# Optimization experiments

Hardware: AMD Instinct MI355X
Metric: run time of the kernel (lower is better)

Reference implementation:

```python
import jax, jax.numpy as jnp
import numpy as np

B, T, C, H = 8, 1024, 1024, 16
D = C // H  # head_dim = 64


def setup_inputs() -> dict:
    key = jax.random.key(0)
    k1, k2, k3 = jax.random.split(key, 3)
    x = jax.random.normal(k1, (B, T, C), dtype=jnp.float32)
    # boolean causal mask: True = attend (PyTorch SDPA bool-mask semantics)
    attn_mask = jnp.tril(jnp.ones((T, T), dtype=jnp.bool_))[None, None, :, :]
    w_attn = jax.random.normal(k2, (C, 3 * C), dtype=jnp.float32) * (1.0 / np.sqrt(C))
    b_attn = jnp.zeros((3 * C,), dtype=jnp.float32)
    w_proj = jax.random.normal(k3, (C, C), dtype=jnp.float32) * (1.0 / np.sqrt(C))
    b_proj = jnp.zeros((C,), dtype=jnp.float32)
    return {"x": x, "attn_mask": attn_mask, "w_attn": w_attn, "b_attn": b_attn,
            "w_proj": w_proj, "b_proj": b_proj}


def reference(x, attn_mask, w_attn, b_attn, w_proj, b_proj):
    Bx, Tx, Cx = x.shape
    qkv = x @ w_attn + b_attn                      # [B,T,3C]
    q, k, v = jnp.split(qkv, 3, axis=-1)
    # [B,T,C] -> [B,H,T,D]
    q = q.reshape(Bx, Tx, H, D).transpose(0, 2, 1, 3)
    k = k.reshape(Bx, Tx, H, D).transpose(0, 2, 1, 3)
    v = v.reshape(Bx, Tx, H, D).transpose(0, 2, 1, 3)
    scale = 1.0 / jnp.sqrt(jnp.asarray(D, dtype=x.dtype))
    scores = jnp.einsum('bhqd,bhkd->bhqk', q, k) * scale  # [B,H,T,T]
    neg = jnp.asarray(jnp.finfo(x.dtype).min, dtype=x.dtype)
    scores = jnp.where(attn_mask, scores, neg)
    probs = jax.nn.softmax(scores, axis=-1)
    y = jnp.einsum('bhqk,bhkd->bhqd', probs, v)    # [B,H,T,D]
    y = y.transpose(0, 2, 1, 3).reshape(Bx, Tx, Cx)
    return y @ w_proj + b_proj
```

## Files before the change

kernel.cpp:

```cpp
#include <hip/hip_runtime.h>


typedef __bf16 bf16x8 __attribute__((ext_vector_type(8)));
typedef float f32x4 __attribute__((ext_vector_type(4)));
typedef unsigned uint4e __attribute__((ext_vector_type(4)));
typedef unsigned short ushort8e __attribute__((ext_vector_type(8)));

typedef __attribute__((address_space(1))) const unsigned as1_u32;
typedef __attribute__((address_space(3))) unsigned as3_u32;

#define NEG_INF (-__builtin_inff())

__device__ __forceinline__ unsigned short f2bf(float f) {
  unsigned u = __builtin_bit_cast(unsigned, f);
  u += 0x7fffu + ((u >> 16) & 1u);
  return (unsigned short)(u >> 16);
}


__global__ void cvt_x_kernel(const float* __restrict__ in, unsigned short* __restrict__ out) {
  size_t i = (size_t)(blockIdx.x * 256 + threadIdx.x) * 8;
  float4 a = *(const float4*)(in + i);
  float4 b = *(const float4*)(in + i + 4);
  ushort8e o;
  o[0] = f2bf(a.x); o[1] = f2bf(a.y); o[2] = f2bf(a.z); o[3] = f2bf(a.w);
  o[4] = f2bf(b.x); o[5] = f2bf(b.y); o[6] = f2bf(b.z); o[7] = f2bf(b.w);
  *(ushort8e*)(out + i) = o;
}

__global__ void cvt_wT_kernel(const float* __restrict__ w, unsigned short* __restrict__ wT,
                              int K, int N) {
  __shared__ float tile[32][33];
  const int n0 = blockIdx.x * 32, k0 = blockIdx.y * 32;
  const int tx = threadIdx.x, ty = threadIdx.y;
#pragma unroll
  for (int i = 0; i < 32; i += 8)
    tile[ty + i][tx] = w[(size_t)(k0 + ty + i) * N + n0 + tx];
  __syncthreads();
#pragma unroll
  for (int i = 0; i < 32; i += 8)
    wT[(size_t)(n0 + ty + i) * K + k0 + tx] = f2bf(tile[tx][ty + i]);
}


template <int EPI, int BNT>
__global__ __launch_bounds__(512, 2) void gemm_kernel(
    const unsigned short* __restrict__ A, const unsigned short* __restrict__ BT,
    const float* __restrict__ bias, float* __restrict__ outF,
    unsigned short* __restrict__ qO, unsigned short* __restrict__ kO,
    unsigned short* __restrict__ vO, int M, int N, int K) {
  constexpr int WN = BNT / 4;
  constexpr int NREP = WN / 16;
  constexpr int BISS = BNT / 64;
  constexpr int ATILE = 256 * 64;
  constexpr int BTILE = BNT * 64;
  __shared__ __align__(16) unsigned short LDS[2][ATILE + BTILE];

  const int tid = threadIdx.x;
  const int w = tid >> 6, lane = tid & 63;
  const int g = lane >> 4, cx = lane & 15;
  const int bm = blockIdx.y * 256, bn = blockIdx.x * BNT;
  const int wm = (w >> 2) * 128;
  const int wn = (w & 3) * WN;
  const int NT = K >> 6;

  const int srow = w * 8 + (lane >> 3);
  const int schunk = ((lane & 7) ^ ((lane >> 3) & 7)) << 3;
  const unsigned short* gAr = A + (size_t)(bm + srow) * K + schunk;
  const unsigned short* gBr = BT + (size_t)(bn + srow) * K + schunk;

  auto stage = [&](int t, int buf) {
    const int ko = t * 64;
#pragma unroll
    for (int i = 0; i < 4; ++i)
      __builtin_amdgcn_global_load_lds(
          (as1_u32*)(const void*)(gAr + (size_t)i * 64 * K + ko),
          (as3_u32*)(void*)&LDS[buf][(i * 64 + w * 8) * 64], 16, 0, 0);
#pragma unroll
    for (int i = 0; i < BISS; ++i)
      __builtin_amdgcn_global_load_lds(
          (as1_u32*)(const void*)(gBr + (size_t)i * 64 * K + ko),
          (as3_u32*)(void*)&LDS[buf][ATILE + (i * 64 + w * 8) * 64], 16, 0, 0);
  };

  f32x4 acc[8][NREP] = {};
  const int rsw = cx & 7;

  stage(0, 0);
  asm volatile("s_waitcnt vmcnt(0)" ::: "memory");
  __builtin_amdgcn_s_barrier();
  asm volatile("" ::: "memory");

  for (int t = 0; t < NT; ++t) {
    const int buf = t & 1;
    if (t + 1 < NT) stage(t + 1, buf ^ 1);
    bf16x8 bfr[NREP][2];
#pragma unroll
    for (int nr = 0; nr < NREP; ++nr) {
      const int RB = wn + nr * 16 + cx;
#pragma unroll
      for (int ks = 0; ks < 2; ++ks)
        bfr[nr][ks] = *(const bf16x8*)&LDS[buf][ATILE + RB * 64 + (((ks * 4 + g) ^ rsw) << 3)];
    }
#pragma unroll
    for (int q = 0; q < 4; ++q) {
      bf16x8 af[2][2];
#pragma unroll
      for (int mr = 0; mr < 2; ++mr) {
        const int R = wm + q * 32 + mr * 16 + cx;
#pragma unroll
        for (int ks = 0; ks < 2; ++ks)
          af[mr][ks] = *(const bf16x8*)&LDS[buf][R * 64 + (((ks * 4 + g) ^ rsw) << 3)];
      }
      __builtin_amdgcn_s_setprio(1);
#pragma unroll
      for (int mr = 0; mr < 2; ++mr)
#pragma unroll
        for (int nr = 0; nr < NREP; ++nr)
#pragma unroll
          for (int ks = 0; ks < 2; ++ks)
            acc[q * 2 + mr][nr] = __builtin_amdgcn_mfma_f32_16x16x32_bf16(
                af[mr][ks], bfr[nr][ks], acc[q * 2 + mr][nr], 0, 0, 0);
      __builtin_amdgcn_s_setprio(0);
    }
    if (t + 1 < NT) {
      asm volatile("s_waitcnt vmcnt(0)" ::: "memory");
      __builtin_amdgcn_s_barrier();
      asm volatile("" ::: "memory");
    }
  }

  if (EPI == 0) {
#pragma unroll
    for (int q = 0; q < 4; ++q)
#pragma unroll
      for (int mr = 0; mr < 2; ++mr) {
        const int m0 = bm + wm + q * 32 + mr * 16 + (g << 2);
        const int b = m0 >> 10, t0 = m0 & 1023;
#pragma unroll
        for (int nr = 0; nr < NREP; ++nr) {
          const int n = bn + wn + nr * 16 + cx;
          const float bv = bias[n];
          const int which = n >> 10, rem = n & 1023;
          const int h = rem >> 6, d = rem & 63;
          const int bh = b * 16 + h;
          f32x4& a4 = acc[q * 2 + mr][nr];
          if (which == 2) {
            uint2 pv;
            pv.x = (unsigned)f2bf(a4[0] + bv) | ((unsigned)f2bf(a4[1] + bv) << 16);
            pv.y = (unsigned)f2bf(a4[2] + bv) | ((unsigned)f2bf(a4[3] + bv) << 16);
            *(uint2*)(vO + ((size_t)bh * 64 + d) * 1024 + t0) = pv;
          } else {
            unsigned short* dst = (which == 0 ? qO : kO);
            const float scl = (which == 0) ? 0.18033688011112042f : 1.0f;
#pragma unroll
            for (int r = 0; r < 4; ++r)
              dst[((size_t)bh * 1024 + (t0 + r)) * 64 + d] = f2bf((a4[r] + bv) * scl);
          }
        }
      }
  } else {
#pragma unroll
    for (int q = 0; q < 4; ++q)
#pragma unroll
      for (int mr = 0; mr < 2; ++mr) {
        const int m0 = bm + wm + q * 32 + mr * 16 + (g << 2);
#pragma unroll
        for (int nr = 0; nr < NREP; ++nr) {
          const int n = bn + wn + nr * 16 + cx;
          const float bv = bias[n];
          f32x4& a4 = acc[q * 2 + mr][nr];
#pragma unroll
          for (int r = 0; r < 4; ++r)
            outF[(size_t)(m0 + r) * N + n] = a4[r] + bv;
        }
      }
  }
}


__global__ __launch_bounds__(256) void attn_kernel(
    const unsigned short* __restrict__ qB, const unsigned short* __restrict__ kB,
    const unsigned short* __restrict__ vB, unsigned short* __restrict__ yB) {
  __shared__ __align__(16) unsigned short Ks[2][64 * 64];
  __shared__ __align__(16) unsigned short Vs[2][64 * 64];
  const int lane = threadIdx.x & 63, w = threadIdx.x >> 6;
  const int g = lane >> 4, cx = lane & 15;
  const int bh = blockIdx.x;
  const int qt = 7 - blockIdx.y;
  const int qb0 = qt * 128;
  const int nt = qt * 2 + 2;
  const unsigned short* Qh = qB + (size_t)bh * 65536;
  const unsigned short* Kh = kB + (size_t)bh * 65536;
  const unsigned short* Vh = vB + (size_t)bh * 65536;

  const int qsb0 = qb0 + w * 16, qsb1 = qb0 + 64 + w * 16;

  bf16x8 qf[2][2];
#pragma unroll
  for (int s = 0; s < 2; ++s) {
    const int qq = (s ? qsb1 : qsb0) + cx;
#pragma unroll
    for (int h = 0; h < 2; ++h)
      qf[s][h] = *(const bf16x8*)(Qh + (size_t)qq * 64 + h * 32 + g * 8);
  }

  f32x4 oacc[2][4] = {};
  float mrun0 = NEG_INF, mrun1 = NEG_INF, L0 = 0.f, L1 = 0.f;

  const int srl = lane >> 3, sch = lane & 7;

  auto stage = [&](int t, int buf) {
#pragma unroll
    for (int i = 0; i < 2; ++i) {
      const int row = w * 16 + i * 8 + srl;
      const int csw = (sch ^ (row & 7)) << 3;
      const unsigned short* gk = Kh + (size_t)(t * 64 + row) * 64 + csw;
      __builtin_amdgcn_global_load_lds((as1_u32*)(const void*)gk,
          (as3_u32*)(void*)&Ks[buf][(w * 16 + i * 8) * 64], 16, 0, 0);
      const unsigned short* gv = Vh + (size_t)row * 1024 + t * 64 + csw;
      __builtin_amdgcn_global_load_lds((as1_u32*)(const void*)gv,
          (as3_u32*)(void*)&Vs[buf][(w * 16 + i * 8) * 64], 16, 0, 0);
    }
  };

  auto mkpf = [&](const float* pp) -> bf16x8 {
    unsigned lo0 = (unsigned)f2bf(pp[0]) | ((unsigned)f2bf(pp[1]) << 16);
    unsigned hi0 = (unsigned)f2bf(pp[2]) | ((unsigned)f2bf(pp[3]) << 16);
    unsigned lo1 = (unsigned)f2bf(pp[4]) | ((unsigned)f2bf(pp[5]) << 16);
    unsigned hi1 = (unsigned)f2bf(pp[6]) | ((unsigned)f2bf(pp[7]) << 16);
    const int s0 = ((g & 1) << 5) + cx, s1 = s0 + 16;
    unsigned a0 = __shfl(lo0, s0), a1 = __shfl(hi0, s0), a2 = __shfl(lo0, s1), a3 = __shfl(hi0, s1);
    unsigned b0 = __shfl(lo1, s0), b1 = __shfl(hi1, s0), b2 = __shfl(lo1, s1), b3 = __shfl(hi1, s1);
    const bool chh = g >= 2;
    uint4e pw;
    pw[0] = chh ? b0 : a0; pw[1] = chh ? b1 : a1; pw[2] = chh ? b2 : a2; pw[3] = chh ? b3 : a3;
    return __builtin_bit_cast(bf16x8, pw);
  };

  stage(0, 0);
  asm volatile("s_waitcnt vmcnt(0)" ::: "memory");
  __builtin_amdgcn_s_barrier();
  asm volatile("" ::: "memory");

  for (int t = 0; t < nt; ++t) {
    const int buf = t & 1;
    if (t + 1 < nt) stage(t + 1, buf ^ 1);
    const int k0 = t * 64;
    const bool act0 = k0 <= qsb0 + 15;

    bf16x8 kf[4][2];
#pragma unroll
    for (int kc = 0; kc < 4; ++kc) {
      const int row = kc * 16 + cx;
#pragma unroll
      for (int h = 0; h < 2; ++h)
        kf[kc][h] = *(const bf16x8*)&Ks[buf][row * 64 + (((h * 4 + g) ^ (row & 7)) << 3)];
    }
    f32x4 sa[2][4];
#pragma unroll
    for (int kc = 0; kc < 4; ++kc) {
      f32x4 z = {0.f, 0.f, 0.f, 0.f};
      sa[1][kc] = __builtin_amdgcn_mfma_f32_16x16x32_bf16(kf[kc][0], qf[1][0], z, 0, 0, 0);
      sa[1][kc] = __builtin_amdgcn_mfma_f32_16x16x32_bf16(kf[kc][1], qf[1][1], sa[1][kc], 0, 0, 0);
    }
    if (act0) {
#pragma unroll
      for (int kc = 0; kc < 4; ++kc) {
        f32x4 z = {0.f, 0.f, 0.f, 0.f};
        sa[0][kc] = __builtin_amdgcn_mfma_f32_16x16x32_bf16(kf[kc][0], qf[0][0], z, 0, 0, 0);
        sa[0][kc] = __builtin_amdgcn_mfma_f32_16x16x32_bf16(kf[kc][1], qf[0][1], sa[0][kc], 0, 0, 0);
      }
    }

    bf16x8 vf[4][2];
#pragma unroll
    for (int db = 0; db < 4; ++db) {
      const int row = db * 16 + cx;
#pragma unroll
      for (int h = 0; h < 2; ++h)
        vf[db][h] = *(const bf16x8*)&Vs[buf][row * 64 + (((h * 4 + g) ^ (row & 7)) << 3)];
    }

#pragma unroll
    for (int s = 0; s < 2; ++s) {
      if (s == 0 && !act0) continue;
      const int qsb = s ? qsb1 : qsb0;
      const int qg = qsb + cx;
      float& mrun = s ? mrun1 : mrun0;
      float& L = s ? L1 : L0;
      float p[16];
      const bool straddle = (k0 + 63) > qsb;
#pragma unroll
      for (int kc = 0; kc < 4; ++kc)
#pragma unroll
        for (int r = 0; r < 4; ++r) {
          float v = sa[s][kc][r];
          if (straddle && (k0 + kc * 16 + (g << 2) + r) > qg) v = NEG_INF;
          p[kc * 4 + r] = v;
        }
      float m01 = fmaxf(fmaxf(p[0], p[1]), fmaxf(p[2], p[3]));
      float m23 = fmaxf(fmaxf(p[4], p[5]), fmaxf(p[6], p[7]));
      float m45 = fmaxf(fmaxf(p[8], p[9]), fmaxf(p[10], p[11]));
      float m67 = fmaxf(fmaxf(p[12], p[13]), fmaxf(p[14], p[15]));
      float pm = fmaxf(fmaxf(m01, m23), fmaxf(m45, m67));
      pm = fmaxf(pm, __shfl_xor(pm, 16));
      pm = fmaxf(pm, __shfl_xor(pm, 32));
      const float mnew = fmaxf(mrun, pm);
      const float cs = __builtin_amdgcn_exp2f(mrun - mnew);
      mrun = mnew;
      float ps = 0.f;
#pragma unroll
      for (int e = 0; e < 16; ++e) {
        p[e] = __builtin_amdgcn_exp2f(p[e] - mnew);
        ps += p[e];
      }
      ps += __shfl_xor(ps, 16);
      ps += __shfl_xor(ps, 32);
      L = L * cs + ps;
#pragma unroll
      for (int db = 0; db < 4; ++db) {
        oacc[s][db][0] *= cs; oacc[s][db][1] *= cs;
        oacc[s][db][2] *= cs; oacc[s][db][3] *= cs;
      }
      const bf16x8 pf0 = mkpf(p);
      const bf16x8 pf1 = mkpf(p + 8);
#pragma unroll
      for (int db = 0; db < 4; ++db) {
        oacc[s][db] = __builtin_amdgcn_mfma_f32_16x16x32_bf16(vf[db][0], pf0, oacc[s][db], 0, 0, 0);
        oacc[s][db] = __builtin_amdgcn_mfma_f32_16x16x32_bf16(vf[db][1], pf1, oacc[s][db], 0, 0, 0);
      }
    }

    asm volatile("s_waitcnt vmcnt(0)" ::: "memory");
    __builtin_amdgcn_s_barrier();
    asm volatile("" ::: "memory");
  }

  const int b = bh >> 4, h = bh & 15;
#pragma unroll
  for (int s = 0; s < 2; ++s) {
    const float inv = 1.0f / (s ? L1 : L0);
    const int qg = (s ? qsb1 : qsb0) + cx;
    unsigned short* yp = yB + (size_t)(b * 1024 + qg) * 1024 + h * 64;
#pragma unroll
    for (int db = 0; db < 4; ++db) {
      uint2 pv;
      pv.x = (unsigned)f2bf(oacc[s][db][0] * inv) | ((unsigned)f2bf(oacc[s][db][1] * inv) << 16);
      pv.y = (unsigned)f2bf(oacc[s][db][2] * inv) | ((unsigned)f2bf(oacc[s][db][3] * inv) << 16);
      *(uint2*)(yp + db * 16 + (g << 2)) = pv;
    }
  }
}


extern "C" void kernel_launch(void* const* d_in, const int* in_sizes, int n_in,
                              void* d_out, int out_size, void* d_ws, size_t ws_size,
                              hipStream_t stream) {
  (void)in_sizes; (void)n_in; (void)out_size; (void)ws_size;
  const float* x = (const float*)d_in[0];
  const float* w_attn = (const float*)d_in[2];
  const float* b_attn = (const float*)d_in[3];
  const float* w_proj = (const float*)d_in[4];
  const float* b_proj = (const float*)d_in[5];
  float* out = (float*)d_out;

  char* ws = (char*)d_ws;
  unsigned short* xb     = (unsigned short*)(ws);
  unsigned short* wqkvT  = (unsigned short*)(ws + 16777216);
  unsigned short* wprojT = (unsigned short*)(ws + 23068672);
  unsigned short* qb     = (unsigned short*)(ws + 25165824);
  unsigned short* kb     = (unsigned short*)(ws + 41943040);
  unsigned short* vtb    = (unsigned short*)(ws + 58720256);
  unsigned short* yb     = (unsigned short*)(ws + 75497472);

  cvt_x_kernel<<<4096, 256, 0, stream>>>(x, xb);
  cvt_wT_kernel<<<dim3(96, 32), dim3(32, 8), 0, stream>>>(w_attn, wqkvT, 1024, 3072);
  cvt_wT_kernel<<<dim3(32, 32), dim3(32, 8), 0, stream>>>(w_proj, wprojT, 1024, 1024);

  gemm_kernel<0, 256><<<dim3(12, 32), 512, 0, stream>>>(xb, wqkvT, b_attn, nullptr,
                                                        qb, kb, vtb, 8192, 3072, 1024);
  attn_kernel<<<dim3(128, 8), 256, 0, stream>>>(qb, kb, vtb, yb);
  gemm_kernel<1, 128><<<dim3(8, 32), 512, 0, stream>>>(yb, wprojT, b_proj, out,
                                                       nullptr, nullptr, nullptr, 8192, 1024, 1024);
}
```

Measured before the change: 170.2 us.

## Triple-buffer GEMM K-loop, shrink QKV tile to 128 wide, remap blocks per XCD

Moves the GEMM from double buffering to a three-stage LDS ring with prefetch distance two and a partial vmcnt wait, so global loads overlap compute for longer. The QKV GEMM tile width drops from 256 to 128 (768 blocks) and a 1D grid is remapped so consecutive tiles land on the same XCD for L2 reuse. The trip count is hardcoded to 16, so K is fixed at 1024. LDS use grows to three buffers, which may limit occupancy, and each block does less work per B tile.

```diff
diff --git a/kernel.cpp b/kernel.cpp
--- a/kernel.cpp
+++ b/kernel.cpp
@@ -43,33 +43,36 @@
 }
 
 
-template <int EPI, int BNT>
+template <int EPI, int NTN>
 __global__ __launch_bounds__(512, 2) void gemm_kernel(
     const unsigned short* __restrict__ A, const unsigned short* __restrict__ BT,
     const float* __restrict__ bias, float* __restrict__ outF,
     unsigned short* __restrict__ qO, unsigned short* __restrict__ kO,
     unsigned short* __restrict__ vO, int M, int N, int K) {
-  constexpr int WN = BNT / 4;
-  constexpr int NREP = WN / 16;
-  constexpr int BISS = BNT / 64;
   constexpr int ATILE = 256 * 64;
-  constexpr int BTILE = BNT * 64;
-  __shared__ __align__(16) unsigned short LDS[2][ATILE + BTILE];
+  constexpr int BTILE = 128 * 64;
+  constexpr int NT = 16;
+  __shared__ __align__(16) unsigned short LDS[3][ATILE + BTILE];
 
   const int tid = threadIdx.x;
   const int w = tid >> 6, lane = tid & 63;
   const int g = lane >> 4, cx = lane & 15;
-  const int bm = blockIdx.y * 256, bn = blockIdx.x * BNT;
+
+  constexpr int CPX = NTN * 32 / 8;
+  const int bid = blockIdx.x;
+  const int wg = (bid & 7) * CPX + (bid >> 3);
+  const int bm = (wg / NTN) * 256, bn = (wg % NTN) * 128;
+
   const int wm = (w >> 2) * 128;
-  const int wn = (w & 3) * WN;
-  const int NT = K >> 6;
+  const int wn = (w & 3) * 32;
 
   const int srow = w * 8 + (lane >> 3);
   const int schunk = ((lane & 7) ^ ((lane >> 3) & 7)) << 3;
   const unsigned short* gAr = A + (size_t)(bm + srow) * K + schunk;
   const unsigned short* gBr = BT + (size_t)(bn + srow) * K + schunk;
 
-  auto stage = [&](int t, int buf) {
+  auto stage = [&](int t) {
+    const int buf = t % 3;
     const int ko = t * 64;
 #pragma unroll
     for (int i = 0; i < 4; ++i)
@@ -77,30 +80,33 @@
           (as1_u32*)(const void*)(gAr + (size_t)i * 64 * K + ko),
           (as3_u32*)(void*)&LDS[buf][(i * 64 + w * 8) * 64], 16, 0, 0);
 #pragma unroll
-    for (int i = 0; i < BISS; ++i)
+    for (int i = 0; i < 2; ++i)
       __builtin_amdgcn_global_load_lds(
           (as1_u32*)(const void*)(gBr + (size_t)i * 64 * K + ko),
           (as3_u32*)(void*)&LDS[buf][ATILE + (i * 64 + w * 8) * 64], 16, 0, 0);
   };
 
-  f32x4 acc[8][NREP] = {};
+  f32x4 acc[8][2] = {};
   const int rsw = cx & 7;
 
-  stage(0, 0);
-  asm volatile("s_waitcnt vmcnt(0)" ::: "memory");
-  __builtin_amdgcn_s_barrier();
-  asm volatile("" ::: "memory");
+  stage(0);
+  stage(1);
 
   for (int t = 0; t < NT; ++t) {
-    const int buf = t & 1;
-    if (t + 1 < NT) stage(t + 1, buf ^ 1);
-    bf16x8 bfr[NREP][2];
-#pragma unroll
-    for (int nr = 0; nr < NREP; ++nr) {
+    if (t + 1 < NT) asm volatile("s_waitcnt vmcnt(6)" ::: "memory");
+    else            asm volatile("s_waitcnt vmcnt(0)" ::: "memory");
+    __builtin_amdgcn_s_barrier();
+    asm volatile("" ::: "memory");
+    if (t + 2 < NT) stage(t + 2);
+
+    const unsigned short* Lb = LDS[t % 3];
+    bf16x8 bfr[2][2];
+#pragma unroll
+    for (int nr = 0; nr < 2; ++nr) {
       const int RB = wn + nr * 16 + cx;
 #pragma unroll
       for (int ks = 0; ks < 2; ++ks)
-        bfr[nr][ks] = *(const bf16x8*)&LDS[buf][ATILE + RB * 64 + (((ks * 4 + g) ^ rsw) << 3)];
+        bfr[nr][ks] = *(const bf16x8*)&Lb[ATILE + RB * 64 + (((ks * 4 + g) ^ rsw) << 3)];
     }
 #pragma unroll
     for (int q = 0; q < 4; ++q) {
@@ -110,24 +116,21 @@
         const int R = wm + q * 32 + mr * 16 + cx;
 #pragma unroll
         for (int ks = 0; ks < 2; ++ks)
-          af[mr][ks] = *(const bf16x8*)&LDS[buf][R * 64 + (((ks * 4 + g) ^ rsw) << 3)];
+          af[mr][ks] = *(const bf16x8*)&Lb[R * 64 + (((ks * 4 + g) ^ rsw) << 3)];
       }
       __builtin_amdgcn_s_setprio(1);
 #pragma unroll
       for (int mr = 0; mr < 2; ++mr)
 #pragma unroll
-        for (int nr = 0; nr < NREP; ++nr)
+        for (int nr = 0; nr < 2; ++nr)
 #pragma unroll
           for (int ks = 0; ks < 2; ++ks)
             acc[q * 2 + mr][nr] = __builtin_amdgcn_mfma_f32_16x16x32_bf16(
                 af[mr][ks], bfr[nr][ks], acc[q * 2 + mr][nr], 0, 0, 0);
       __builtin_amdgcn_s_setprio(0);
     }
-    if (t + 1 < NT) {
-      asm volatile("s_waitcnt vmcnt(0)" ::: "memory");
-      __builtin_amdgcn_s_barrier();
-      asm volatile("" ::: "memory");
-    }
+    __builtin_amdgcn_s_barrier();
+    asm volatile("" ::: "memory");
   }
 
   if (EPI == 0) {
@@ -138,7 +141,7 @@
         const int m0 = bm + wm + q * 32 + mr * 16 + (g << 2);
         const int b = m0 >> 10, t0 = m0 & 1023;
 #pragma unroll
-        for (int nr = 0; nr < NREP; ++nr) {
+        for (int nr = 0; nr < 2; ++nr) {
           const int n = bn + wn + nr * 16 + cx;
           const float bv = bias[n];
           const int which = n >> 10, rem = n & 1023;
@@ -166,7 +169,7 @@
       for (int mr = 0; mr < 2; ++mr) {
         const int m0 = bm + wm + q * 32 + mr * 16 + (g << 2);
 #pragma unroll
-        for (int nr = 0; nr < NREP; ++nr) {
+        for (int nr = 0; nr < 2; ++nr) {
           const int n = bn + wn + nr * 16 + cx;
           const float bv = bias[n];
           f32x4& a4 = acc[q * 2 + mr][nr];
@@ -378,9 +381,9 @@
   cvt_wT_kernel<<<dim3(96, 32), dim3(32, 8), 0, stream>>>(w_attn, wqkvT, 1024, 3072);
   cvt_wT_kernel<<<dim3(32, 32), dim3(32, 8), 0, stream>>>(w_proj, wprojT, 1024, 1024);
 
-  gemm_kernel<0, 256><<<dim3(12, 32), 512, 0, stream>>>(xb, wqkvT, b_attn, nullptr,
-                                                        qb, kb, vtb, 8192, 3072, 1024);
+  gemm_kernel<0, 24><<<768, 512, 0, stream>>>(xb, wqkvT, b_attn, nullptr,
+                                              qb, kb, vtb, 8192, 3072, 1024);
   attn_kernel<<<dim3(128, 8), 256, 0, stream>>>(qb, kb, vtb, yb);
-  gemm_kernel<1, 128><<<dim3(8, 32), 512, 0, stream>>>(yb, wprojT, b_proj, out,
-                                                       nullptr, nullptr, nullptr, 8192, 1024, 1024);
-}
+  gemm_kernel<1, 8><<<256, 512, 0, stream>>>(yb, wprojT, b_proj, out,
+                                             nullptr, nullptr, nullptr, 8192, 1024, 1024);
+}
```

Result: no change. 167.4 us (-1.6%).
